# Kernel tuning notes

Hardware: AMD Instinct MI355X
Metric: run time of the kernel (lower is better)

## Reference

```python
import jax, jax.numpy as jnp
import numpy as np

EPS = 1e-6

def _layernorm(x):
    mu = jnp.mean(x, axis=-1, keepdims=True)
    var = jnp.mean(jnp.square(x - mu), axis=-1, keepdims=True)
    return (x - mu) / jnp.sqrt(var + EPS)

def setup_inputs() -> dict:
    key = jax.random.key(0)
    ks = jax.random.split(key, 12)
    B, N, C = 4, 1024, 1024
    H = 16
    Dff = 4 * C
    s = 0.02
    x = jax.random.normal(ks[0], (B, N, C), dtype=jnp.float32)
    mask = jax.random.randint(ks[1], (N, N), 0, 2) > 0  # True = attend
    wq = jax.random.normal(ks[2], (C, C), dtype=jnp.float32) * s
    bq = jnp.zeros((C,), dtype=jnp.float32)
    wkv = jax.random.normal(ks[3], (C, 2 * C), dtype=jnp.float32) * s
    bkv = jnp.zeros((2 * C,), dtype=jnp.float32)
    wo = jax.random.normal(ks[4], (C, C), dtype=jnp.float32) * s
    bo = jnp.zeros((C,), dtype=jnp.float32)
    w1 = jax.random.normal(ks[5], (C, Dff), dtype=jnp.float32) * s
    b1 = jnp.zeros((Dff,), dtype=jnp.float32)
    w2 = jax.random.normal(ks[6], (Dff, C), dtype=jnp.float32) * s
    b2 = jnp.zeros((C,), dtype=jnp.float32)
    return {"x": x, "mask": mask, "wq": wq, "bq": bq, "wkv": wkv, "bkv": bkv,
            "wo": wo, "bo": bo, "w1": w1, "b1": b1, "w2": w2, "b2": b2}

def reference(x, mask, wq, bq, wkv, bkv, wo, bo, w1, b1, w2, b2):
    B, N, C = x.shape
    H = 16
    d = C // H
    scale = d ** -0.5
    max_neg = -jnp.finfo(x.dtype).max
    # attn_bias: 0 where mask True, -max where False; broadcast [1,1,N,N]
    attn_bias = jnp.where(mask, jnp.asarray(0.0, x.dtype), jnp.asarray(max_neg, x.dtype))[None, None]

    # --- pre-norm attention ---
    xn = _layernorm(x)
    q = (xn @ wq + bq).reshape(B, N, H, d)
    kv = xn @ wkv + bkv
    k, v = jnp.split(kv, 2, axis=-1)
    k = k.reshape(B, N, H, d)
    v = v.reshape(B, N, H, d)
    sim = jnp.einsum('bihd,bjhd->bhij', q, k) * scale + attn_bias
    attn = jax.nn.softmax(sim, axis=-1)
    o = jnp.einsum('bhij,bjhd->bihd', attn, v).reshape(B, N, C)
    x = x + (o @ wo + bo)

    # --- pre-norm MLP with tanh-approx GELU ---
    xn = _layernorm(x)
    h = jax.nn.gelu(xn @ w1 + b1, approximate=True)
    x = x + (h @ w2 + b2)
    return x
```

## Files before the change

kernel.cpp:

```cpp
#include <hip/hip_runtime.h>
#include <hip/hip_bf16.h>

typedef short bf16x8 __attribute__((ext_vector_type(8)));
typedef float f32x4 __attribute__((ext_vector_type(4)));
typedef unsigned short u16x8 __attribute__((ext_vector_type(8)));

#define MFMA16(a,b,c) __builtin_amdgcn_mfma_f32_16x16x32_bf16((a),(b),(c),0,0,0)

__device__ inline unsigned short f32_to_bf16(float f){
  union { float f; unsigned u; } v; v.f = f;
  unsigned u = v.u;
  u += 0x7FFFu + ((u >> 16) & 1u);
  return (unsigned short)(u >> 16);
}
__device__ inline float bf16_to_f32(unsigned short u){
  union { unsigned u; float f; } v; v.u = ((unsigned)u)<<16; return v.f;
}

__device__ inline float gelu_fast(float x){
  const float c1 = -2.302118484f;
  const float c2 = -0.102944227f;
  float p = __builtin_amdgcn_exp2f(x*__builtin_fmaf(c2, x*x, c1));
  return x*__builtin_amdgcn_rcpf(1.0f + p);
}

__device__ inline void gload16(const void* g, void* l){
  __builtin_amdgcn_global_load_lds(
      (const __attribute__((address_space(1))) void*)g,
      (__attribute__((address_space(3))) void*)l, 16, 0, 0);
}

__device__ inline int xcd_swz(int lin, int nwg){
  int cpx = nwg >> 3;
  return (lin & 7)*cpx + (lin >> 3);
}

__global__ void detect_mask_kernel(const unsigned* __restrict__ m, int* __restrict__ flag){
  __shared__ int s;
  if (threadIdx.x == 0) s = 0;
  __syncthreads();
  unsigned w = m[threadIdx.x];
  if (w > 1u) atomicOr(&s, 1);
  __syncthreads();
  if (threadIdx.x == 0) *flag = s;
}

__global__ __launch_bounds__(256) void mask_bias_kernel(
    const void* __restrict__ mask, const int* __restrict__ flag,
    unsigned short* __restrict__ biasr){
  __shared__ float mt[16][64];
  int qg = blockIdx.x, jt = blockIdx.y;
  int t = threadIdx.x;
  int fl = *flag;
  int jc = jt*64 + (t&63);
  #pragma unroll
  for (int k2=0;k2<4;k2++){
    int qr = qg*16 + (t>>6) + k2*4;
    bool a = fl ? (((const unsigned char*)mask)[(size_t)qr*1024 + jc] != 0)
                : (((const int*)mask)[(size_t)qr*1024 + jc] != 0);
    mt[(t>>6)+k2*4][t&63] = a ? -23.083120654223414f : -1e30f;
  }
  __syncthreads();
  ushort4 ob;
  unsigned short tmp[4];
  #pragma unroll
  for (int u=0;u<4;u++){
    int p = t*4+u;
    int e = p&15, lane = p>>4;
    int i = e>>2, jj = e&3;
    int ln2 = lane&15, g2 = lane>>4;
    tmp[u] = f32_to_bf16(mt[g2*4+i][jj*16+ln2]);
  }
  ob.x=tmp[0]; ob.y=tmp[1]; ob.z=tmp[2]; ob.w=tmp[3];
  *(ushort4*)&biasr[((size_t)(qg*16+jt)*64)*16 + t*4] = ob;
}

__global__ __launch_bounds__(256) void transpose_cvt_kernel(
    const float* __restrict__ W, unsigned short* __restrict__ WT, int K, int N){
  __shared__ float tile[32][37];
  int n0 = blockIdx.x*32, k0 = blockIdx.y*32;
  int r = threadIdx.x>>3, c4 = threadIdx.x&7;
  float4 v = *(const float4*)&W[(size_t)(k0+r)*N + n0 + c4*4];
  tile[r][c4*4+0]=v.x; tile[r][c4*4+1]=v.y; tile[r][c4*4+2]=v.z; tile[r][c4*4+3]=v.w;
  __syncthreads();
  ushort4 o;
  o.x = f32_to_bf16(tile[c4*4+0][r]);
  o.y = f32_to_bf16(tile[c4*4+1][r]);
  o.z = f32_to_bf16(tile[c4*4+2][r]);
  o.w = f32_to_bf16(tile[c4*4+3][r]);
  *(ushort4*)&WT[(size_t)(n0+r)*K + k0 + c4*4] = o;
}

__global__ __launch_bounds__(256) void vtrans_kernel(
    const unsigned short* __restrict__ qkv, unsigned short* __restrict__ vt){
  __shared__ unsigned short t[32][33];
  int b = blockIdx.z;
  int n0 = blockIdx.x*32, d0 = blockIdx.y*32;
  int tx = threadIdx.x & 31, ty = threadIdx.x >> 5;
  #pragma unroll
  for (int r=0;r<4;r++)
    t[ty+8*r][tx] = qkv[(size_t)(b*1024 + n0+ty+8*r)*3072 + 2048 + d0+tx];
  __syncthreads();
  #pragma unroll
  for (int r=0;r<4;r++)
    vt[((size_t)b<<20) + (size_t)(d0+ty+8*r)*1024 + n0+tx] = t[tx][ty+8*r];
}

__global__ void bias_concat_kernel(const float* __restrict__ bq,
                                   const float* __restrict__ bkv,
                                   float* __restrict__ dst){
  int i = blockIdx.x*256 + threadIdx.x;
  if (i < 3072) dst[i] = (i < 1024) ? bq[i] : bkv[i-1024];
}

__global__ __launch_bounds__(256) void ln_kernel(const float* __restrict__ x,
                                                 unsigned short* __restrict__ xn){
  const int C = 1024;
  size_t row = blockIdx.x;
  float4 v = reinterpret_cast<const float4*>(x + row*C)[threadIdx.x];
  float s = v.x+v.y+v.z+v.w;
  float q = v.x*v.x+v.y*v.y+v.z*v.z+v.w*v.w;
  #pragma unroll
  for (int off=32; off; off>>=1){ s += __shfl_xor(s,off); q += __shfl_xor(q,off); }
  __shared__ float sm[8];
  int wv = threadIdx.x>>6, ln = threadIdx.x&63;
  if (ln==0){ sm[wv]=s; sm[4+wv]=q; }
  __syncthreads();
  float S = sm[0]+sm[1]+sm[2]+sm[3];
  float Q = sm[4]+sm[5]+sm[6]+sm[7];
  float mu  = S*(1.0f/1024.0f);
  float var = Q*(1.0f/1024.0f) - mu*mu;
  float inv = rsqrtf(var + 1e-6f);
  ushort4 o;
  o.x = f32_to_bf16((v.x-mu)*inv);
  o.y = f32_to_bf16((v.y-mu)*inv);
  o.z = f32_to_bf16((v.z-mu)*inv);
  o.w = f32_to_bf16((v.w-mu)*inv);
  reinterpret_cast<ushort4*>(xn + row*C)[threadIdx.x] = o;
}

template<int EPI>
__global__ __launch_bounds__(256) void gemm128_kernel(
    const unsigned short* __restrict__ A,
    const unsigned short* __restrict__ BT,
    const float* __restrict__ bias,
    const float* __restrict__ resid,
    void* __restrict__ Cout,
    int M, int N, int K)
{
  __shared__ __align__(16) unsigned short lds[3][8192];
  int tid = threadIdx.x, wave = tid>>6, lane = tid&63;
  int nbx = gridDim.x;
  int lin = blockIdx.y*nbx + blockIdx.x;
  int w = xcd_swz(lin, nbx*gridDim.y);
  int m0 = (w/nbx)*128, n0 = (w%nbx)*128;
  int ln = lane&15, g = lane>>4;
  int wm = wave>>1, wn = wave&1;

  const unsigned short* sA[2];
  const unsigned short* sB[2];
  #pragma unroll
  for (int p=0;p<2;p++){
    int idx = p*256 + tid;
    int row = idx>>2, c = idx&3;
    int ch = c ^ ((row>>1)&3);
    sA[p] = A  + (size_t)(m0+row)*K + ch*8;
    sB[p] = BT + (size_t)(n0+row)*K + ch*8;
  }

  f32x4 acc[4][4] = {};
  int nt = K/32;
  const int rdsw = (g ^ ((ln>>1)&3))*8;

  auto STAGE = [&](int t, int buf){
    int ko = t*32;
    #pragma unroll
    for (int p=0;p<2;p++)
      gload16(sA[p]+ko, (char*)&lds[buf][0]    + (p*256 + wave*64)*16);
    #pragma unroll
    for (int p=0;p<2;p++)
      gload16(sB[p]+ko, (char*)&lds[buf][4096] + (p*256 + wave*64)*16);
  };

  STAGE(0,0); STAGE(1,1); STAGE(2,2);

  int cb = 0;
  for (int t=0; t<nt; ++t){
    int rem = nt-1-t;
    if (rem >= 2)      asm volatile("s_waitcnt vmcnt(8)" ::: "memory");
    else if (rem == 1) asm volatile("s_waitcnt vmcnt(4)" ::: "memory");
    else               asm volatile("s_waitcnt vmcnt(0)" ::: "memory");
    __builtin_amdgcn_s_barrier();

    const unsigned short* lb = lds[cb];
    bf16x8 a[4], b[4];
    #pragma unroll
    for (int mi=0;mi<4;mi++)
      a[mi] = *(const bf16x8*)(lb + (wm*64+mi*16+ln)*32 + rdsw);
    #pragma unroll
    for (int ni=0;ni<4;ni++)
      b[ni] = *(const bf16x8*)(lb + 4096 + (wn*64+ni*16+ln)*32 + rdsw);
    #pragma unroll
    for (int mi=0;mi<4;mi++)
      #pragma unroll
      for (int ni=0;ni<4;ni++)
        acc[mi][ni] = MFMA16(a[mi], b[ni], acc[mi][ni]);

    asm volatile("s_waitcnt lgkmcnt(0)" ::: "memory");
    __builtin_amdgcn_s_barrier();
    if (t+3 < nt) STAGE(t+3, cb);
    cb = (cb==2) ? 0 : cb+1;
  }

  #pragma unroll
  for (int mi=0;mi<4;mi++){
    int r0 = m0 + wm*64 + mi*16 + g*4;
    #pragma unroll
    for (int ni=0;ni<4;ni++){
      int c = n0 + wn*64 + ni*16 + ln;
      float bs = bias[c];
      f32x4 cc = acc[mi][ni];
      #pragma unroll
      for (int i=0;i<4;i++){
        int r = r0 + i;
        float v = cc[i] + bs;
        if (EPI == 1){
          v += resid[(size_t)r*N + c];
          ((float*)Cout)[(size_t)r*N + c] = v;
        } else if (EPI == 2){
          ((unsigned short*)Cout)[(size_t)r*N + c] = f32_to_bf16(gelu_fast(v));
        } else {
          ((unsigned short*)Cout)[(size_t)r*N + c] = f32_to_bf16(v);
        }
      }
    }
  }
}

template<int EPI>
__global__ __launch_bounds__(512) void gemm8_kernel(
    const unsigned short* __restrict__ A,
    const unsigned short* __restrict__ BT,
    const float* __restrict__ bias,
    void* __restrict__ Cout,
    int M, int N, int K)
{
  extern __shared__ __align__(16) char smem[];
  const int tid = threadIdx.x, wave = tid>>6, lane = tid&63;
  const int ln = lane&15, g = lane>>4;
  const int wm = wave>>2, wn = wave&3;
  const int nbx = gridDim.x;
  const int lin = blockIdx.y*nbx + blockIdx.x;
  const int wsw = xcd_swz(lin, nbx*gridDim.y);
  const int m0 = (wsw/nbx)*256, n0 = (wsw%nbx)*256;
  const int NT = K>>6;
  const int axor = ((g ^ ((ln>>1)&3))<<4);

  auto STAGE = [&](int kt, int h){
    const bool isB = h&1; const int kh = h>>1;
    const unsigned short* src = isB ? BT : A;
    const int base0 = isB ? n0 : m0;
    char* region = smem + (isB?65536:0) + (kt&1)*32768 + kh*16384;
    #pragma unroll
    for (int r=0;r<2;r++){
      int idx = r*512 + tid;
      int row = idx>>2;
      int col = kt*64 + kh*32 + ((((idx&3) ^ ((row>>1)&3))<<4)>>1);
      gload16(src + (size_t)(base0+row)*K + col,
              region + (r*512 + wave*64)*16);
    }
  };

  STAGE(0,0); STAGE(0,1); STAGE(0,2); STAGE(0,3);
  STAGE(1,0); STAGE(1,1); STAGE(1,2);
  asm volatile("s_waitcnt vmcnt(6)" ::: "memory");
  __builtin_amdgcn_s_barrier();
  __builtin_amdgcn_sched_barrier(0);

  f32x4 acc[8][4] = {};
  bf16x8 a[8], b[2];

  for (int t=0; t<NT; ++t){
    const int cur = t&1;
    char* Ac0 = smem + cur*32768;
    char* Ac1 = Ac0 + 16384;
    char* Bc0 = smem + 65536 + cur*32768;
    char* Bc1 = Bc0 + 16384;
    #pragma unroll
    for (int mi=0;mi<8;mi++)
      a[mi] = *(const bf16x8*)(Ac0 + (wm*128+mi*16+ln)*64 + axor);
    b[0] = *(const bf16x8*)(Bc0 + (wn*64+ 0+ln)*64 + axor);
    b[1] = *(const bf16x8*)(Bc0 + (wn*64+16+ln)*64 + axor);
    if (t+1 < NT) STAGE(t+1,3);
    __builtin_amdgcn_s_barrier();
    __builtin_amdgcn_s_setprio(1);
    #pragma unroll
    for (int mi=0;mi<8;mi++){
      acc[mi][0] = MFMA16(a[mi], b[0], acc[mi][0]);
      acc[mi][1] = MFMA16(a[mi], b[1], acc[mi][1]);
    }
    __builtin_amdgcn_s_setprio(0);
    __builtin_amdgcn_s_barrier();
    b[0] = *(const bf16x8*)(Bc0 + (wn*64+32+ln)*64 + axor);
    b[1] = *(const bf16x8*)(Bc0 + (wn*64+48+ln)*64 + axor);
    if (t+2 < NT) STAGE(t+2,0);
    __builtin_amdgcn_s_barrier();
    __builtin_amdgcn_s_setprio(1);
    #pragma unroll
    for (int mi=0;mi<8;mi++){
      acc[mi][2] = MFMA16(a[mi], b[0], acc[mi][2]);
      acc[mi][3] = MFMA16(a[mi], b[1], acc[mi][3]);
    }
    __builtin_amdgcn_s_setprio(0);
    __builtin_amdgcn_s_barrier();
    #pragma unroll
    for (int mi=0;mi<8;mi++)
      a[mi] = *(const bf16x8*)(Ac1 + (wm*128+mi*16+ln)*64 + axor);
    b[0] = *(const bf16x8*)(Bc1 + (wn*64+ 0+ln)*64 + axor);
    b[1] = *(const bf16x8*)(Bc1 + (wn*64+16+ln)*64 + axor);
    if (t+2 < NT) STAGE(t+2,1);
    __builtin_amdgcn_s_barrier();
    __builtin_amdgcn_s_setprio(1);
    #pragma unroll
    for (int mi=0;mi<8;mi++){
      acc[mi][0] = MFMA16(a[mi], b[0], acc[mi][0]);
      acc[mi][1] = MFMA16(a[mi], b[1], acc[mi][1]);
    }
    __builtin_amdgcn_s_setprio(0);
    __builtin_amdgcn_s_barrier();
    b[0] = *(const bf16x8*)(Bc1 + (wn*64+32+ln)*64 + axor);
    b[1] = *(const bf16x8*)(Bc1 + (wn*64+48+ln)*64 + axor);
    if (t+2 < NT) STAGE(t+2,2);
    __builtin_amdgcn_s_barrier();
    __builtin_amdgcn_s_setprio(1);
    #pragma unroll
    for (int mi=0;mi<8;mi++){
      acc[mi][2] = MFMA16(a[mi], b[0], acc[mi][2]);
      acc[mi][3] = MFMA16(a[mi], b[1], acc[mi][3]);
    }
    __builtin_amdgcn_s_setprio(0);
    if (t+2 < NT) asm volatile("s_waitcnt vmcnt(6)" ::: "memory");
    else          asm volatile("s_waitcnt vmcnt(0)" ::: "memory");
    __builtin_amdgcn_s_barrier();
    __builtin_amdgcn_sched_barrier(0);
  }

  #pragma unroll
  for (int mi=0;mi<8;mi++){
    int r0 = m0 + wm*128 + mi*16 + g*4;
    #pragma unroll
    for (int nj=0;nj<4;nj++){
      int c = n0 + wn*64 + nj*16 + ln;
      float bs = bias[c];
      f32x4 cc = acc[mi][nj];
      #pragma unroll
      for (int i=0;i<4;i++){
        int r = r0 + i;
        float v = cc[i] + bs;
        if (EPI == 2){
          ((unsigned short*)Cout)[(size_t)r*N + c] = f32_to_bf16(gelu_fast(v));
        } else {
          ((unsigned short*)Cout)[(size_t)r*N + c] = f32_to_bf16(v);
        }
      }
    }
  }
}

__global__ __launch_bounds__(256,6) void attn_kernel(
    const unsigned short* __restrict__ qkv,
    const unsigned short* __restrict__ vt,
    const unsigned short* __restrict__ biasr,
    unsigned short* __restrict__ pn,
    float* __restrict__ lsumg)
{
  const int N = 1024, NK = 3072;
  const float SCL = 0.18033688011112042f;
  __shared__ __align__(16) unsigned short lK[64*64];
  __shared__ __align__(16) unsigned short lV[64*64];
  __shared__ __align__(16) unsigned short plds[4][16][72];
  int bh = blockIdx.x, qt = blockIdx.y, sp = blockIdx.z;
  int b = bh>>4, h = bh&15;
  int tid = threadIdx.x, wave = tid>>6, lane = tid&63;
  int ln = lane&15, g = lane>>4;
  size_t base = (size_t)b*N;
  int q_local = qt*64 + wave*16;

  const unsigned short* qptr = qkv + (base + q_local + ln)*NK + h*64;
  bf16x8 aq0 = *(const bf16x8*)(qptr + g*8);
  bf16x8 aq1 = *(const bf16x8*)(qptr + 32 + g*8);

  int r0s = tid>>3,        c0 = (tid&7) ^ (r0s&7);
  int r1s = 32 + (tid>>3), c1 = (tid&7) ^ (r1s&7);
  const unsigned short* kg0 = qkv + (base + r0s)*NK + 1024 + h*64 + c0*8;
  const unsigned short* kg1 = qkv + (base + r1s)*NK + 1024 + h*64 + c1*8;
  const unsigned short* vg0 = vt + ((size_t)b<<20) + (size_t)(h*64 + r0s)*N + c0*8;
  const unsigned short* vg1 = vt + ((size_t)b<<20) + (size_t)(h*64 + r1s)*N + c1*8;
  char* lKd0 = (char*)lK + (wave*64)*16;
  char* lKd1 = (char*)lK + (256 + wave*64)*16;
  char* lVd0 = (char*)lV + (wave*64)*16;
  char* lVd1 = (char*)lV + (256 + wave*64)*16;

  const unsigned short* brp = biasr +
      (((size_t)(qt*4 + wave)*16)*64 + lane)*16;

  f32x4 oacc[4] = {};
  float lsum[4] = {0.f,0.f,0.f,0.f};
  const int xl = (ln&7);

  for (int t=0; t<8; ++t){
    int j0 = sp*512 + t*64;
    __syncthreads();
    gload16(kg0 + (size_t)j0*NK, lKd0);
    gload16(kg1 + (size_t)j0*NK, lKd1);
    gload16(vg0 + j0, lVd0);
    gload16(vg1 + j0, lVd1);
    int jt = j0>>6;
    bf16x8 bb0 = *(const bf16x8*)(brp + (size_t)jt*1024);
    bf16x8 bb1 = *(const bf16x8*)(brp + (size_t)jt*1024 + 8);
    asm volatile("s_waitcnt vmcnt(0)" ::: "memory");
    __builtin_amdgcn_s_barrier();

    f32x4 s[4];
    #pragma unroll
    for (int jj=0;jj<4;jj++){
      int row = jj*16+ln;
      bf16x8 k0 = *(const bf16x8*)((const char*)lK + row*128 + ((g^xl)<<4));
      bf16x8 k1 = *(const bf16x8*)((const char*)lK + row*128 + (((g+4)^xl)<<4));
      s[jj] = (f32x4){};
      s[jj] = MFMA16(aq0, k0, s[jj]);
      s[jj] = MFMA16(aq1, k1, s[jj]);
    }
    #pragma unroll
    for (int i=0;i<4;i++){
      #pragma unroll
      for (int jj=0;jj<4;jj++){
        int e = i*4+jj;
        unsigned short bu = (e<8) ? (unsigned short)bb0[e] : (unsigned short)bb1[e-8];
        float ev = exp2f(fmaf(s[jj][i], SCL, bf16_to_f32(bu)));
        lsum[i] += ev;
        plds[wave][4*g+i][jj*16+ln] = f32_to_bf16(ev);
      }
    }
    asm volatile("s_waitcnt lgkmcnt(0)" ::: "memory");
    __builtin_amdgcn_sched_barrier(0);
    bf16x8 p0 = *(const bf16x8*)&plds[wave][ln][g*8];
    bf16x8 p1 = *(const bf16x8*)&plds[wave][ln][32 + g*8];
    #pragma unroll
    for (int nd=0;nd<4;nd++){
      int row = nd*16+ln;
      bf16x8 v0 = *(const bf16x8*)((const char*)lV + row*128 + ((g^xl)<<4));
      bf16x8 v1 = *(const bf16x8*)((const char*)lV + row*128 + (((g+4)^xl)<<4));
      oacc[nd] = MFMA16(p0, v0, oacc[nd]);
      oacc[nd] = MFMA16(p1, v1, oacc[nd]);
    }
  }

  #pragma unroll
  for (int i=0;i<4;i++){
    float l = lsum[i];
    l += __shfl_xor(l,1); l += __shfl_xor(l,2);
    l += __shfl_xor(l,4); l += __shfl_xor(l,8);
    if (ln == 0)
      lsumg[((size_t)sp<<16) + (size_t)(base + q_local + 4*g + i)*16 + h] = l;
  }
  #pragma unroll
  for (int nd=0;nd<4;nd++){
    #pragma unroll
    for (int i=0;i<4;i++){
      int qr = q_local + 4*g + i;
      pn[((size_t)sp<<22) + (base+qr)*1024 + h*64 + nd*16 + ln] = f32_to_bf16(oacc[nd][i]);
    }
  }
}

__global__ __launch_bounds__(256) void attn_reduce_kernel(
    const unsigned short* __restrict__ pn,
    const float* __restrict__ lsumg,
    unsigned short* __restrict__ o)
{
  size_t idx = ((size_t)blockIdx.x*256 + threadIdx.x)*8;
  int r = (int)(idx>>10);
  int h = (int)((idx&1023)>>6);
  float inv = 1.0f/(lsumg[(size_t)r*16+h] + lsumg[(1u<<16) + (size_t)r*16+h]);
  u16x8 p0 = *(const u16x8*)(pn + idx);
  u16x8 p1 = *(const u16x8*)(pn + (1u<<22) + idx);
  u16x8 res;
  #pragma unroll
  for (int e=0;e<8;e++)
    res[e] = f32_to_bf16((bf16_to_f32((unsigned short)p0[e]) +
                          bf16_to_f32((unsigned short)p1[e]))*inv);
  *(u16x8*)(o + idx) = res;
}

extern "C" void kernel_launch(void* const* d_in, const int* in_sizes, int n_in,
                              void* d_out, int out_size, void* d_ws, size_t ws_size,
                              hipStream_t stream)
{
  (void)in_sizes; (void)n_in; (void)out_size; (void)ws_size;
  const float* x   = (const float*)d_in[0];
  const void*  mask= d_in[1];
  const float* wq  = (const float*)d_in[2];
  const float* bq  = (const float*)d_in[3];
  const float* wkv = (const float*)d_in[4];
  const float* bkv = (const float*)d_in[5];
  const float* wo  = (const float*)d_in[6];
  const float* bo  = (const float*)d_in[7];
  const float* w1  = (const float*)d_in[8];
  const float* b1  = (const float*)d_in[9];
  const float* w2  = (const float*)d_in[10];
  const float* b2  = (const float*)d_in[11];
  float* out = (float*)d_out;

  char* ws = (char*)d_ws;
  size_t off = 0;
  auto alloc = [&](size_t bytes){ size_t o = off; off += (bytes + 255) & ~(size_t)255; return o; };
  unsigned short* WqkvT = (unsigned short*)(ws + alloc(3072u*1024u*2));
  unsigned short* WoT   = (unsigned short*)(ws + alloc(1024u*1024u*2));
  unsigned short* W1T   = (unsigned short*)(ws + alloc(4096u*1024u*2));
  unsigned short* W2T   = (unsigned short*)(ws + alloc(1024u*4096u*2));
  float*          BIASQ = (float*)(ws + alloc(3072u*4));
  int*            FLAG  = (int*)(ws + alloc(256));
  float*          LSUM  = (float*)(ws + alloc(2u*4096u*16u*4));
  unsigned short* BIASR = (unsigned short*)(ws + alloc(64u*16u*64u*16u*2));
  unsigned short* XN    = (unsigned short*)(ws + alloc(4096u*1024u*2));
  float*          X1    = (float*)(ws + alloc(4096u*1024u*4));
  unsigned short* QKV   = (unsigned short*)(ws + alloc(4096u*4096u*2));
  unsigned short* VT    = QKV + (size_t)4096u*3072u;
  unsigned short* PN    = (unsigned short*)X1;

  hipFuncSetAttribute(reinterpret_cast<const void*>(&gemm8_kernel<0>),
                      hipFuncAttributeMaxDynamicSharedMemorySize, 131072);

  transpose_cvt_kernel<<<dim3(32,32),  256, 0, stream>>>(wq,  WqkvT,               1024, 1024);
  transpose_cvt_kernel<<<dim3(64,32),  256, 0, stream>>>(wkv, WqkvT + 1024u*1024u, 1024, 2048);
  transpose_cvt_kernel<<<dim3(32,32),  256, 0, stream>>>(wo,  WoT,                 1024, 1024);
  transpose_cvt_kernel<<<dim3(128,32), 256, 0, stream>>>(w1,  W1T,                 1024, 4096);
  transpose_cvt_kernel<<<dim3(32,128), 256, 0, stream>>>(w2,  W2T,                 4096, 1024);
  bias_concat_kernel<<<12, 256, 0, stream>>>(bq, bkv, BIASQ);
  detect_mask_kernel<<<1, 256, 0, stream>>>((const unsigned*)mask, FLAG);
  mask_bias_kernel<<<dim3(64,16), 256, 0, stream>>>(mask, FLAG, BIASR);

  ln_kernel<<<4096, 256, 0, stream>>>(x, XN);
  gemm8_kernel<0><<<dim3(12,16), 512, 131072, stream>>>(XN, WqkvT, BIASQ, QKV, 4096, 3072, 1024);
  vtrans_kernel<<<dim3(32,32,4), 256, 0, stream>>>(QKV, VT);
  attn_kernel<<<dim3(64,16,2), 256, 0, stream>>>(QKV, VT, BIASR, PN, LSUM);
  attn_reduce_kernel<<<2048, 256, 0, stream>>>(PN, LSUM, XN);
  gemm128_kernel<1><<<dim3(8,32), 256, 0, stream>>>(XN, WoT, bo, x, X1, 4096, 1024, 1024);
  ln_kernel<<<4096, 256, 0, stream>>>(X1, XN);
  gemm128_kernel<2><<<dim3(32,32), 256, 0, stream>>>(XN, W1T, b1, nullptr, QKV, 4096, 4096, 1024);
  gemm128_kernel<1><<<dim3(8,32), 256, 0, stream>>>(QKV, W2T, b2, X1, out, 4096, 1024, 4096);
}
```

Measured before the change: 239.9 us.

## Split-K the MLP down-projection GEMM into two halves with a reduce kernel

The final 4096x1024x4096 GEMM previously ran on only 256 blocks with a long K loop. It is now split along K into two z-slices, giving 512 blocks. Slice 0 writes bias plus residual plus partial sum in fp32 to the output, and slice 1 writes its partial to a bf16 plane reusing the XN buffer. A new elementwise kernel then adds the bf16 partial into the output. This raises GPU occupancy at the cost of an extra launch, extra memory traffic, and bf16 rounding of half the accumulation.

```diff
diff --git a/kernel.cpp b/kernel.cpp
--- a/kernel.cpp
+++ b/kernel.cpp
@@ -146,7 +146,8 @@
     const float* __restrict__ bias,
     const float* __restrict__ resid,
     void* __restrict__ Cout,
-    int M, int N, int K)
+    unsigned short* __restrict__ plane,
+    int M, int N, int K, int Ksp)
 {
   __shared__ __align__(16) unsigned short lds[3][8192];
   int tid = threadIdx.x, wave = tid>>6, lane = tid&63;
@@ -154,6 +155,7 @@
   int lin = blockIdx.y*nbx + blockIdx.x;
   int w = xcd_swz(lin, nbx*gridDim.y);
   int m0 = (w/nbx)*128, n0 = (w%nbx)*128;
+  int kbase = (EPI==3) ? blockIdx.z*Ksp : 0;
   int ln = lane&15, g = lane>>4;
   int wm = wave>>1, wn = wave&1;
 
@@ -164,12 +166,12 @@
     int idx = p*256 + tid;
     int row = idx>>2, c = idx&3;
     int ch = c ^ ((row>>1)&3);
-    sA[p] = A  + (size_t)(m0+row)*K + ch*8;
-    sB[p] = BT + (size_t)(n0+row)*K + ch*8;
+    sA[p] = A  + (size_t)(m0+row)*K + kbase + ch*8;
+    sB[p] = BT + (size_t)(n0+row)*K + kbase + ch*8;
   }
 
   f32x4 acc[4][4] = {};
-  int nt = K/32;
+  int nt = Ksp/32;
   const int rdsw = (g ^ ((ln>>1)&3))*8;
 
   auto STAGE = [&](int t, int buf){
@@ -218,23 +220,44 @@
     #pragma unroll
     for (int ni=0;ni<4;ni++){
       int c = n0 + wn*64 + ni*16 + ln;
-      float bs = bias[c];
       f32x4 cc = acc[mi][ni];
       #pragma unroll
       for (int i=0;i<4;i++){
         int r = r0 + i;
-        float v = cc[i] + bs;
-        if (EPI == 1){
-          v += resid[(size_t)r*N + c];
-          ((float*)Cout)[(size_t)r*N + c] = v;
+        if (EPI == 3){
+          if (blockIdx.z == 0)
+            ((float*)Cout)[(size_t)r*N + c] = cc[i] + bias[c] + resid[(size_t)r*N + c];
+          else
+            plane[(size_t)r*N + c] = f32_to_bf16(cc[i]);
+        } else if (EPI == 1){
+          ((float*)Cout)[(size_t)r*N + c] = cc[i] + bias[c] + resid[(size_t)r*N + c];
         } else if (EPI == 2){
-          ((unsigned short*)Cout)[(size_t)r*N + c] = f32_to_bf16(gelu_fast(v));
+          ((unsigned short*)Cout)[(size_t)r*N + c] = f32_to_bf16(gelu_fast(cc[i] + bias[c]));
         } else {
-          ((unsigned short*)Cout)[(size_t)r*N + c] = f32_to_bf16(v);
+          ((unsigned short*)Cout)[(size_t)r*N + c] = f32_to_bf16(cc[i] + bias[c]);
         }
       }
     }
   }
+}
+
+__global__ __launch_bounds__(256) void mlp2_reduce_kernel(
+    float* __restrict__ out, const unsigned short* __restrict__ p1)
+{
+  size_t i8 = ((size_t)blockIdx.x*256 + threadIdx.x)*8;
+  float4 o0 = *(const float4*)(out + i8);
+  float4 o1 = *(const float4*)(out + i8 + 4);
+  u16x8 a = *(const u16x8*)(p1 + i8);
+  o0.x += bf16_to_f32((unsigned short)a[0]);
+  o0.y += bf16_to_f32((unsigned short)a[1]);
+  o0.z += bf16_to_f32((unsigned short)a[2]);
+  o0.w += bf16_to_f32((unsigned short)a[3]);
+  o1.x += bf16_to_f32((unsigned short)a[4]);
+  o1.y += bf16_to_f32((unsigned short)a[5]);
+  o1.z += bf16_to_f32((unsigned short)a[6]);
+  o1.w += bf16_to_f32((unsigned short)a[7]);
+  *(float4*)(out + i8) = o0;
+  *(float4*)(out + i8 + 4) = o1;
 }
 
 template<int EPI>
@@ -528,6 +551,7 @@
   unsigned short* QKV   = (unsigned short*)(ws + alloc(4096u*4096u*2));
   unsigned short* VT    = QKV + (size_t)4096u*3072u;
   unsigned short* PN    = (unsigned short*)X1;
+  unsigned short* PL1   = XN;
 
   hipFuncSetAttribute(reinterpret_cast<const void*>(&gemm8_kernel<0>),
                       hipFuncAttributeMaxDynamicSharedMemorySize, 131072);
@@ -546,8 +570,12 @@
   vtrans_kernel<<<dim3(32,32,4), 256, 0, stream>>>(QKV, VT);
   attn_kernel<<<dim3(64,16,2), 256, 0, stream>>>(QKV, VT, BIASR, PN, LSUM);
   attn_reduce_kernel<<<2048, 256, 0, stream>>>(PN, LSUM, XN);
-  gemm128_kernel<1><<<dim3(8,32), 256, 0, stream>>>(XN, WoT, bo, x, X1, 4096, 1024, 1024);
+  gemm128_kernel<1><<<dim3(8,32), 256, 0, stream>>>(
+      XN, WoT, bo, x, X1, nullptr, 4096, 1024, 1024, 1024);
   ln_kernel<<<4096, 256, 0, stream>>>(X1, XN);
-  gemm128_kernel<2><<<dim3(32,32), 256, 0, stream>>>(XN, W1T, b1, nullptr, QKV, 4096, 4096, 1024);
-  gemm128_kernel<1><<<dim3(8,32), 256, 0, stream>>>(QKV, W2T, b2, X1, out, 4096, 1024, 4096);
-}
+  gemm128_kernel<2><<<dim3(32,32), 256, 0, stream>>>(
+      XN, W1T, b1, nullptr, QKV, nullptr, 4096, 4096, 1024, 1024);
+  gemm128_kernel<3><<<dim3(8,32,2), 256, 0, stream>>>(
+      QKV, W2T, b2, X1, out, PL1, 4096, 1024, 4096, 2048);
+  mlp2_reduce_kernel<<<2048, 256, 0, stream>>>(out, PL1);
+}
```

Result: slower. 251.4 us (+4.8%).

## Double-buffer K/V tiles in attention kernel to overlap loads with compute

Applied to the files above, without the earlier changes.

The attention kernel now keeps two LDS buffers for K and V and issues the global-to-LDS loads for the next key tile before computing on the current one. It waits only on the older loads (vmcnt(4)) and adds a trailing barrier after the PV MFMAs so the buffer being refilled is no longer in use. This hides global load latency behind the QK/softmax/PV work. The cost is double the K/V LDS footprint, and launch bounds drop from 6 to 3 blocks per CU, which reduces occupancy. The vmcnt count also assumes the bias vector loads are ordered with the staged loads.

```diff
diff --git a/kernel.cpp b/kernel.cpp
--- a/kernel.cpp
+++ b/kernel.cpp
@@ -367,7 +367,7 @@
   }
 }
 
-__global__ __launch_bounds__(256,6) void attn_kernel(
+__global__ __launch_bounds__(256,3) void attn_kernel(
     const unsigned short* __restrict__ qkv,
     const unsigned short* __restrict__ vt,
     const unsigned short* __restrict__ biasr,
@@ -376,8 +376,8 @@
 {
   const int N = 1024, NK = 3072;
   const float SCL = 0.18033688011112042f;
-  __shared__ __align__(16) unsigned short lK[64*64];
-  __shared__ __align__(16) unsigned short lV[64*64];
+  __shared__ __align__(16) unsigned short lK[2][4096];
+  __shared__ __align__(16) unsigned short lV[2][4096];
   __shared__ __align__(16) unsigned short plds[4][16][72];
   int bh = blockIdx.x, qt = blockIdx.y, sp = blockIdx.z;
   int b = bh>>4, h = bh&15;
@@ -396,10 +396,6 @@
   const unsigned short* kg1 = qkv + (base + r1s)*NK + 1024 + h*64 + c1*8;
   const unsigned short* vg0 = vt + ((size_t)b<<20) + (size_t)(h*64 + r0s)*N + c0*8;
   const unsigned short* vg1 = vt + ((size_t)b<<20) + (size_t)(h*64 + r1s)*N + c1*8;
-  char* lKd0 = (char*)lK + (wave*64)*16;
-  char* lKd1 = (char*)lK + (256 + wave*64)*16;
-  char* lVd0 = (char*)lV + (wave*64)*16;
-  char* lVd1 = (char*)lV + (256 + wave*64)*16;
 
   const unsigned short* brp = biasr +
       (((size_t)(qt*4 + wave)*16)*64 + lane)*16;
@@ -408,25 +404,33 @@
   float lsum[4] = {0.f,0.f,0.f,0.f};
   const int xl = (ln&7);
 
+  auto STAGE = [&](int t, int buf){
+    int j0 = sp*512 + t*64;
+    gload16(kg0 + (size_t)j0*NK, (char*)lK[buf] + (wave*64)*16);
+    gload16(kg1 + (size_t)j0*NK, (char*)lK[buf] + (256 + wave*64)*16);
+    gload16(vg0 + j0,            (char*)lV[buf] + (wave*64)*16);
+    gload16(vg1 + j0,            (char*)lV[buf] + (256 + wave*64)*16);
+  };
+
+  STAGE(0,0);
+
   for (int t=0; t<8; ++t){
-    int j0 = sp*512 + t*64;
-    __syncthreads();
-    gload16(kg0 + (size_t)j0*NK, lKd0);
-    gload16(kg1 + (size_t)j0*NK, lKd1);
-    gload16(vg0 + j0, lVd0);
-    gload16(vg1 + j0, lVd1);
-    int jt = j0>>6;
+    int jt = sp*8 + t;
     bf16x8 bb0 = *(const bf16x8*)(brp + (size_t)jt*1024);
     bf16x8 bb1 = *(const bf16x8*)(brp + (size_t)jt*1024 + 8);
-    asm volatile("s_waitcnt vmcnt(0)" ::: "memory");
-    __builtin_amdgcn_s_barrier();
-
+    if (t+1 < 8) STAGE(t+1, (t+1)&1);
+    if (t+1 < 8) asm volatile("s_waitcnt vmcnt(4)" ::: "memory");
+    else         asm volatile("s_waitcnt vmcnt(0)" ::: "memory");
+    __builtin_amdgcn_s_barrier();
+
+    const unsigned short* cK = lK[t&1];
+    const unsigned short* cV = lV[t&1];
     f32x4 s[4];
     #pragma unroll
     for (int jj=0;jj<4;jj++){
       int row = jj*16+ln;
-      bf16x8 k0 = *(const bf16x8*)((const char*)lK + row*128 + ((g^xl)<<4));
-      bf16x8 k1 = *(const bf16x8*)((const char*)lK + row*128 + (((g+4)^xl)<<4));
+      bf16x8 k0 = *(const bf16x8*)((const char*)cK + row*128 + ((g^xl)<<4));
+      bf16x8 k1 = *(const bf16x8*)((const char*)cK + row*128 + (((g+4)^xl)<<4));
       s[jj] = (f32x4){};
       s[jj] = MFMA16(aq0, k0, s[jj]);
       s[jj] = MFMA16(aq1, k1, s[jj]);
@@ -449,11 +453,13 @@
     #pragma unroll
     for (int nd=0;nd<4;nd++){
       int row = nd*16+ln;
-      bf16x8 v0 = *(const bf16x8*)((const char*)lV + row*128 + ((g^xl)<<4));
-      bf16x8 v1 = *(const bf16x8*)((const char*)lV + row*128 + (((g+4)^xl)<<4));
+      bf16x8 v0 = *(const bf16x8*)((const char*)cV + row*128 + ((g^xl)<<4));
+      bf16x8 v1 = *(const bf16x8*)((const char*)cV + row*128 + (((g+4)^xl)<<4));
       oacc[nd] = MFMA16(p0, v0, oacc[nd]);
       oacc[nd] = MFMA16(p1, v1, oacc[nd]);
     }
+    asm volatile("s_waitcnt lgkmcnt(0)" ::: "memory");
+    __builtin_amdgcn_s_barrier();
   }
 
   #pragma unroll
```

New measurement: 243.4 us. Within noise of the previous version (+1.4%).
